# Optimization experiments

Hardware: AMD Instinct MI355X
Metric: run time of the kernel (lower is better)

## Reference

```python
import jax, jax.numpy as jnp
import numpy as np

N_NODES = 50000
N_EDGES = 800000
N_GRAPHS = 256
IN_CH = 128
HID = 256
FFN = 256
OUT = 1


def xavier(key, shape):
    fan_in, fan_out = shape[0], shape[1]
    a = jnp.sqrt(6.0 / (fan_in + fan_out))
    return jax.random.uniform(key, shape, jnp.float32, -a, a)


def setup_inputs() -> dict:
    key = jax.random.key(0)
    ks = jax.random.split(key, 12)
    x = jax.random.normal(ks[0], (N_NODES, IN_CH), jnp.float32)
    edge_index = jax.random.randint(ks[1], (2, N_EDGES), 0, N_NODES, jnp.int32)
    batch = jnp.sort(jax.random.randint(ks[2], (N_NODES,), 0, N_GRAPHS, jnp.int32))
    return {
        "x": x,
        "edge_index": edge_index,
        "batch": batch,
        # GCNConv layers (glorot weight, zero bias as in PyG reset_parameters)
        "W1": xavier(ks[3], (IN_CH, HID)), "b1": jnp.zeros((HID,), jnp.float32),
        "W2": xavier(ks[4], (HID, HID)),   "b2": jnp.zeros((HID,), jnp.float32),
        "W3": xavier(ks[5], (HID, HID)),   "b3": jnp.zeros((HID,), jnp.float32),
        # FFN: Linear(HID, FFN) then final Linear(FFN, OUT)
        "Wf": xavier(ks[6], (HID, FFN)),   "bf": jnp.zeros((FFN,), jnp.float32),
        "Wo": xavier(ks[7], (FFN, OUT)),   "bo": jnp.zeros((OUT,), jnp.float32),
    }


def _gcn_norm(edge_index, n_nodes):
    # add self-loops, compute symmetric normalization D^-1/2 (A+I) D^-1/2
    loops = jnp.arange(n_nodes, dtype=edge_index.dtype)
    row = jnp.concatenate([edge_index[0], loops])
    col = jnp.concatenate([edge_index[1], loops])
    deg = jax.ops.segment_sum(jnp.ones_like(col, jnp.float32), col, num_segments=n_nodes)
    dis = jnp.where(deg > 0, jax.lax.rsqrt(jnp.maximum(deg, 1.0)), 0.0)
    norm = dis[row] * dis[col]  # [E+N]
    return row, col, norm


def _gcn_conv(x, W, b, row, col, norm, n_nodes):
    xw = x @ W                                   # [N, H]
    msg = xw[row] * norm[:, None]                # gather + scale  [E+N, H]
    out = jax.ops.segment_sum(msg, col, num_segments=n_nodes)
    return out + b


def reference(x, edge_index, batch, W1, b1, W2, b2, W3, b3, Wf, bf, Wo, bo):
    row, col, norm = _gcn_norm(edge_index, N_NODES)
    h = jax.nn.relu(_gcn_conv(x, W1, b1, row, col, norm, N_NODES))
    h = jax.nn.relu(_gcn_conv(h, W2, b2, row, col, norm, N_NODES))
    h = jax.nn.relu(_gcn_conv(h, W3, b3, row, col, norm, N_NODES))
    # global mean pool over graphs
    counts = jax.ops.segment_sum(jnp.ones((N_NODES,), jnp.float32), batch, num_segments=N_GRAPHS)
    pooled = jax.ops.segment_sum(h, batch, num_segments=N_GRAPHS) / jnp.maximum(counts, 1.0)[:, None]
    # FFN (dropout is identity in eval mode): Linear -> ReLU -> final Linear
    g = jax.nn.relu(pooled @ Wf + bf)
    out = g @ Wo + bo
    return out
```

## Files before the change

kernel.cpp:

```cpp
#include <hip/hip_runtime.h>
#include <hip/hip_bf16.h>
#include <hip/hip_fp16.h>


#define THREADS 256
#define EPB 2048

typedef _Float16 f16x8 __attribute__((ext_vector_type(8)));
typedef float    f32x4 __attribute__((ext_vector_type(4)));
typedef unsigned short u16x8 __attribute__((ext_vector_type(8)));


__global__ void degree_goff_kernel(const int* __restrict__ col, int* __restrict__ deg, int E,
                                   const int* __restrict__ batch, int* __restrict__ goff,
                                   int N, int G) {
    int i = blockIdx.x * THREADS + threadIdx.x;
    if (i < E) atomicAdd(&deg[col[i]], 1);
    if (i < N) {
        int b1 = batch[i];
        int b0 = (i == 0) ? -1 : batch[i - 1];
        for (int g = b0 + 1; g <= b1; ++g) goff[g] = i;
        if (i == N - 1) {
            for (int g = b1 + 1; g <= G; ++g) goff[g] = N;
        }
    }
}

__global__ __launch_bounds__(256) void scanA_kernel(
    const int* __restrict__ in, int* __restrict__ out, int* __restrict__ bsum,
    float* __restrict__ dis, int n) {
    __shared__ int wsum[4];
    int i0 = blockIdx.x * 1024 + threadIdx.x * 4;
    int lane = threadIdx.x & 63, wid = threadIdx.x >> 6;
    int v0 = 0, v1 = 0, v2 = 0, v3 = 0;
    if (i0 + 3 < n) {
        int4 v = *(const int4*)&in[i0];
        v0 = v.x; v1 = v.y; v2 = v.z; v3 = v.w;
    } else {
        if (i0 + 0 < n) v0 = in[i0 + 0];
        if (i0 + 1 < n) v1 = in[i0 + 1];
        if (i0 + 2 < n) v2 = in[i0 + 2];
        if (i0 + 3 < n) v3 = in[i0 + 3];
    }
    if (i0 + 0 < n) dis[i0 + 0] = rsqrtf((float)(v0 + 1));
    if (i0 + 1 < n) dis[i0 + 1] = rsqrtf((float)(v1 + 1));
    if (i0 + 2 < n) dis[i0 + 2] = rsqrtf((float)(v2 + 1));
    if (i0 + 3 < n) dis[i0 + 3] = rsqrtf((float)(v3 + 1));
    v0 = (v0 + 7) & ~7; v1 = (v1 + 7) & ~7;
    v2 = (v2 + 7) & ~7; v3 = (v3 + 7) & ~7;
    int s = v0 + v1 + v2 + v3;
    int inc = s;
    #pragma unroll
    for (int d = 1; d < 64; d <<= 1) {
        int t = __shfl_up(inc, d);
        if (lane >= d) inc += t;
    }
    if (lane == 63) wsum[wid] = inc;
    __syncthreads();
    int add = 0;
    for (int w = 0; w < wid; ++w) add += wsum[w];
    int ex = add + inc - s;
    if (i0 + 0 < n) out[i0 + 0] = ex;
    if (i0 + 1 < n) out[i0 + 1] = ex + v0;
    if (i0 + 2 < n) out[i0 + 2] = ex + v0 + v1;
    if (i0 + 3 < n) out[i0 + 3] = ex + v0 + v1 + v2;
    if (threadIdx.x == 255) bsum[blockIdx.x] = add + inc;
}

__global__ void scanB_kernel(int* __restrict__ bsum, int* __restrict__ total_slot, int nb) {
    int lane = threadIdx.x;
    int v = (lane < nb) ? bsum[lane] : 0;
    int inc = v;
    #pragma unroll
    for (int d = 1; d < 64; d <<= 1) {
        int t = __shfl_up(inc, d);
        if (lane >= d) inc += t;
    }
    if (lane < nb) bsum[lane] = inc - v;
    if (lane == 63) *total_slot = inc;
}

__global__ __launch_bounds__(256) void padfill_x_kernel(
    const int* __restrict__ offs, const int* __restrict__ deg,
    unsigned short* __restrict__ srcs, int N) {
    int slice = blockIdx.x & 7;
    int SL = (N + 7) >> 3;
    int node = slice * SL + (int)(blockIdx.x >> 3) * THREADS + threadIdx.x;
    int nhi = min(N, slice * SL + SL);
    if (node >= nhi) return;
    int s = offs[node] + deg[node], e = offs[node + 1];
    for (int i = s; i < e; ++i) srcs[i] = (unsigned short)N;
}

__global__ __launch_bounds__(256) void csr_fill_x_kernel(
    const int* __restrict__ row, const int* __restrict__ col,
    const int* __restrict__ offs, int* __restrict__ deg,
    unsigned short* __restrict__ srcs, int E, int N) {
    int slice = blockIdx.x & 7;
    int SL = (N + 7) >> 3;
    int nlo = slice * SL;
    int nhi = min(N, nlo + SL);
    int e0 = (int)(blockIdx.x >> 3) * EPB + threadIdx.x * 8;
    if (e0 >= E) return;
    if (e0 + 8 <= E) {
        int4 c0 = *(const int4*)&col[e0];
        int4 c1 = *(const int4*)&col[e0 + 4];
        int4 r0 = *(const int4*)&row[e0];
        int4 r1 = *(const int4*)&row[e0 + 4];
        int cs[8] = {c0.x, c0.y, c0.z, c0.w, c1.x, c1.y, c1.z, c1.w};
        int rs[8] = {r0.x, r0.y, r0.z, r0.w, r1.x, r1.y, r1.z, r1.w};
        #pragma unroll
        for (int j = 0; j < 8; ++j) {
            int c = cs[j];
            if (c >= nlo && c < nhi) {
                int old = atomicSub(&deg[c], 1);
                srcs[offs[c] + old - 1] = (unsigned short)rs[j];
            }
        }
    } else {
        for (int j = 0; j < 8 && e0 + j < E; ++j) {
            int c = col[e0 + j];
            if (c >= nlo && c < nhi) {
                int old = atomicSub(&deg[c], 1);
                srcs[offs[c] + old - 1] = (unsigned short)row[e0 + j];
            }
        }
    }
}

__global__ void convert_kernel(
    int* __restrict__ offs, const int* __restrict__ bsum, int Nfix,
    const float* __restrict__ X, const float* __restrict__ dis,
    _Float16* __restrict__ Xs, int total8, int IC,
    const float* __restrict__ W1, _Float16* __restrict__ W1t, int k1,
    const float* __restrict__ W2, _Float16* __restrict__ W2t,
    const float* __restrict__ W3, _Float16* __restrict__ W3t,
    _Float16* __restrict__ Hs) {
    int i = blockIdx.x * THREADS + threadIdx.x;
    if (i < Nfix) {
        offs[i] += bsum[i >> 10];
        return;
    }
    int j = i - Nfix;
    int Ms = Nfix + 1;
    if (j < total8) {
        int idx = j * 8;
        int node = idx / IC;
        int ch0  = idx % IC;
        float d = dis[node];
        float4 a = *(const float4*)&X[idx];
        float4 b = *(const float4*)&X[idx + 4];
        f16x8 o;
        o[0] = (_Float16)(d * a.x); o[1] = (_Float16)(d * a.y);
        o[2] = (_Float16)(d * a.z); o[3] = (_Float16)(d * a.w);
        o[4] = (_Float16)(d * b.x); o[5] = (_Float16)(d * b.y);
        o[6] = (_Float16)(d * b.z); o[7] = (_Float16)(d * b.w);
        int sw = IC >> 3;
        int slice = ch0 / sw, within = ch0 % sw;
        *(f16x8*)&Xs[((size_t)slice * Ms + node) * sw + within] = o;
        return;
    }
    j -= total8;
    int n1 = k1 * 256;
    if (j < n1) {
        int k = j >> 8, n = j & 255;
        W1t[n * k1 + k] = (_Float16)W1[j];
        return;
    }
    j -= n1;
    if (j < 65536) {
        int k = j >> 8, n = j & 255;
        W2t[n * 256 + k] = (_Float16)W2[j];
        return;
    }
    j -= 65536;
    if (j < 65536) {
        int k = j >> 8, n = j & 255;
        W3t[n * 256 + k] = (_Float16)W3[j];
        return;
    }
    j -= 65536;
    {
        int swx = IC >> 3;
        int nx = 8 * swx;
        if (j < nx) {
            int slice = j / swx, wi = j % swx;
            Xs[((size_t)slice * Ms + Nfix) * swx + wi] = (_Float16)0.f;
            return;
        }
        j -= nx;
        if (j < 256) {
            int slice = j >> 5, wi = j & 31;
            Hs[((size_t)slice * Ms + Nfix) * 32 + wi] = (_Float16)0.f;
        }
    }
}


template<int CH>
__global__ __launch_bounds__(256) void aggregate_slice_kernel(
    const _Float16* __restrict__ X, const int* __restrict__ offs,
    const unsigned short* __restrict__ srcs, const float* __restrict__ dis,
    _Float16* __restrict__ A, int N) {
    constexpr int LPN = CH / 64;
    constexpr int NPB = 256 / LPN;
    int bid   = blockIdx.x;
    int slice = bid & 7;
    int tile  = bid >> 3;
    int node  = tile * NPB + threadIdx.x / LPN;
    if (node >= N) return;
    int lane = threadIdx.x % LPN;
    size_t Ms = (size_t)N + 1;
    const f16x8* Xv = (const f16x8*)X + (size_t)slice * Ms * LPN;
    f16x8 self = Xv[(size_t)node * LPN + lane];
    float acc[8], acc2[8];
    #pragma unroll
    for (int j = 0; j < 8; ++j) { acc[j] = (float)self[j]; acc2[j] = 0.f; }
    int s = offs[node], e = offs[node + 1];
    int nit = (e - s) >> 3;
    if (nit > 0) {
        const u16x8* ip = (const u16x8*)&srcs[s];
        u16x8 idx = ip[0];
        for (int it = 0; it < nit; ++it) {
            u16x8 nxt = ip[min(it + 1, nit - 1)];
            f16x8 v0 = Xv[(size_t)idx[0] * LPN + lane];
            f16x8 v1 = Xv[(size_t)idx[1] * LPN + lane];
            f16x8 v2 = Xv[(size_t)idx[2] * LPN + lane];
            f16x8 v3 = Xv[(size_t)idx[3] * LPN + lane];
            f16x8 v4 = Xv[(size_t)idx[4] * LPN + lane];
            f16x8 v5 = Xv[(size_t)idx[5] * LPN + lane];
            f16x8 v6 = Xv[(size_t)idx[6] * LPN + lane];
            f16x8 v7 = Xv[(size_t)idx[7] * LPN + lane];
            #pragma unroll
            for (int j = 0; j < 8; ++j) {
                acc[j]  += ((float)v0[j] + (float)v2[j]) + ((float)v4[j] + (float)v6[j]);
                acc2[j] += ((float)v1[j] + (float)v3[j]) + ((float)v5[j] + (float)v7[j]);
            }
            idx = nxt;
        }
    }
    float dn = dis[node];
    f16x8 o;
    #pragma unroll
    for (int j = 0; j < 8; ++j) o[j] = (_Float16)(dn * (acc[j] + acc2[j]));
    f16x8* Av = (f16x8*)A + (size_t)slice * Ms * LPN;
    __builtin_nontemporal_store(o, &Av[(size_t)node * LPN + lane]);
}


template<int K, int MODE>
__global__ __launch_bounds__(256) void gemm_as_kernel(
    const _Float16* __restrict__ A, const _Float16* __restrict__ Bt,
    const float* __restrict__ bias, const float* __restrict__ dscale,
    _Float16* __restrict__ H, float* __restrict__ pooled,
    const int* __restrict__ batch, int M, int Ms) {
    constexpr int LSA = K + 40;
    constexpr int KC = K / 32;
    constexpr int SPR = K / 8;
    constexpr int SPS = K / 64;
    constexpr int SW  = K / 8;
    __shared__ _Float16 As[64 * LSA];
    int tid = threadIdx.x;
    int m0 = blockIdx.x * 64;

    {
        constexpr int RPI = 256 / SPR;
        int r_in = tid % RPI;
        int seg  = tid / RPI;
        int slice = seg / SPS, sub = seg % SPS;
        #pragma unroll
        for (int it = 0; it < 64 / RPI; ++it) {
            int r = it * RPI + r_in;
            int gr = m0 + r;
            uint4 v = make_uint4(0, 0, 0, 0);
            if (gr < M) v = *(const uint4*)&A[((size_t)slice * Ms + gr) * SW + sub * 8];
            *(uint4*)&As[r * LSA + seg * 8] = v;
        }
    }
    __syncthreads();

    int wid = tid >> 6, lane = tid & 63;
    int l16 = lane & 15, quad = lane >> 4;
    int wn = wid * 64;

    f32x4 acc[4][4] = {};
    const _Float16* Bbase = Bt + (size_t)(wn + l16) * K + quad * 8;

    #pragma unroll
    for (int kc = 0; kc < KC; ++kc) {
        f16x8 bh[4];
        #pragma unroll
        for (int ni = 0; ni < 4; ++ni)
            bh[ni] = *(const f16x8*)&Bbase[(size_t)(ni * 16) * K + kc * 32];
        #pragma unroll
        for (int mi = 0; mi < 4; ++mi) {
            f16x8 ah = *(const f16x8*)&As[(mi * 16 + l16) * LSA + kc * 32 + quad * 8];
            #pragma unroll
            for (int ni = 0; ni < 4; ++ni)
                acc[mi][ni] = __builtin_amdgcn_mfma_f32_16x16x32_f16(ah, bh[ni], acc[mi][ni], 0, 0, 0);
        }
    }

    #pragma unroll
    for (int mi = 0; mi < 4; ++mi) {
        int rbase = m0 + mi * 16;
        int g0 = 0, g15 = 0;
        if (MODE == 2) {
            g0  = batch[min(rbase, M - 1)];
            g15 = batch[min(rbase + 15, M - 1)];
        }
        #pragma unroll
        for (int ni = 0; ni < 4; ++ni) {
            int col = wn + ni * 16 + l16;
            float bv = bias[col];
            if (MODE == 1) {
                size_t hbase = (size_t)(col >> 5) * Ms * 32 + (col & 31);
                #pragma unroll
                for (int r = 0; r < 4; ++r) {
                    int grow = rbase + quad * 4 + r;
                    if (grow < M) {
                        float v = fmaxf(acc[mi][ni][r] + bv, 0.f) * dscale[grow];
                        H[hbase + (size_t)grow * 32] = (_Float16)v;
                    }
                }
            } else {
                if (g0 == g15) {
                    float p = 0.f;
                    #pragma unroll
                    for (int r = 0; r < 4; ++r) {
                        int grow = rbase + quad * 4 + r;
                        float v = fmaxf(acc[mi][ni][r] + bv, 0.f);
                        p += (grow < M) ? v : 0.f;
                    }
                    p += __shfl_xor(p, 16);
                    p += __shfl_xor(p, 32);
                    if (quad == 0) atomicAdd(&pooled[g0 * 256 + col], p);
                } else {
                    #pragma unroll
                    for (int r = 0; r < 4; ++r) {
                        int grow = rbase + quad * 4 + r;
                        if (grow < M) {
                            float v = fmaxf(acc[mi][ni][r] + bv, 0.f);
                            atomicAdd(&pooled[batch[grow] * 256 + col], v);
                        }
                    }
                }
            }
        }
    }
}


__global__ __launch_bounds__(256) void ffn_kernel(
    const float* __restrict__ pooled, const int* __restrict__ goff,
    const float* __restrict__ Wf, const float* __restrict__ bf,
    const float* __restrict__ Wo, const float* __restrict__ bo,
    float* __restrict__ out) {
    __shared__ float p[256];
    __shared__ float red[256];
    int g = blockIdx.x, t = threadIdx.x;
    int cnt = goff[g + 1] - goff[g];
    float inv = 1.f / (float)max(cnt, 1);
    p[t] = pooled[g * 256 + t] * inv;
    __syncthreads();
    float s = bf[t];
    #pragma unroll 8
    for (int k = 0; k < 256; ++k) s = fmaf(p[k], Wf[k * 256 + t], s);
    float gv = fmaxf(s, 0.f);
    red[t] = gv * Wo[t];
    __syncthreads();
    for (int o = 128; o > 0; o >>= 1) {
        if (t < o) red[t] += red[t + o];
        __syncthreads();
    }
    if (t == 0) out[g] = red[0] + bo[0];
}


extern "C" void kernel_launch(void* const* d_in, const int* in_sizes, int n_in,
                              void* d_out, int out_size, void* d_ws, size_t ws_size,
                              hipStream_t stream) {
    const float* x   = (const float*)d_in[0];
    const int*   ei  = (const int*)d_in[1];
    const int*   bat = (const int*)d_in[2];
    const float* W1  = (const float*)d_in[3];
    const float* b1  = (const float*)d_in[4];
    const float* W2  = (const float*)d_in[5];
    const float* b2  = (const float*)d_in[6];
    const float* W3  = (const float*)d_in[7];
    const float* b3  = (const float*)d_in[8];
    const float* Wf  = (const float*)d_in[9];
    const float* bf  = (const float*)d_in[10];
    const float* Wo  = (const float*)d_in[11];
    const float* bo  = (const float*)d_in[12];
    float* out = (float*)d_out;

    const int N  = in_sizes[2];
    const int E  = in_sizes[1] / 2;
    const int IC = in_sizes[0] / N;
    const int HID = 256;
    const int G  = out_size;
    const int Ms = N + 1;
    const int* row = ei;
    const int* col = ei + E;

    char* w = (char*)d_ws;
    size_t off = 0;
    auto alloc = [&](size_t bytes) -> void* {
        void* p = w + off;
        off += (bytes + 255) & ~(size_t)255;
        return p;
    };
    int*   deg    = (int*)alloc((size_t)N * 4);
    float* pooled = (float*)alloc((size_t)G * HID * 4);
    float* dis    = (float*)alloc((size_t)N * 4);
    int*   offs   = (int*)alloc((size_t)(N + 1) * 4);
    unsigned short* srcs = (unsigned short*)alloc(((size_t)E + 7 * (size_t)N + 8) * 2);
    int*   goff   = (int*)alloc((size_t)(G + 1) * 4);
    int*   bsum   = (int*)alloc((size_t)64 * 4);
    _Float16* W1t = (_Float16*)alloc((size_t)HID * IC * 2);
    _Float16* W2t = (_Float16*)alloc((size_t)HID * HID * 2);
    _Float16* W3t = (_Float16*)alloc((size_t)HID * HID * 2);
    _Float16* Xs  = (_Float16*)alloc((size_t)Ms * IC * 2);
    _Float16* Ah  = (_Float16*)alloc((size_t)Ms * HID * 2);
    _Float16* Hs  = (_Float16*)alloc((size_t)Ms * HID * 2);
    (void)ws_size; (void)n_in;

    size_t zlen = (((size_t)N * 4 + 255) & ~(size_t)255) + (size_t)G * HID * 4;
    hipMemsetAsync(deg, 0, zlen, stream);

    int nb = (N + 1023) / 1024;
    degree_goff_kernel<<<(E + THREADS - 1) / THREADS, THREADS, 0, stream>>>(
        col, deg, E, bat, goff, N, G);
    scanA_kernel<<<nb, 256, 0, stream>>>(deg, offs, bsum, dis, N);
    scanB_kernel<<<1, 64, 0, stream>>>(bsum, &offs[N], nb);

    int total8 = N * IC / 8;
    int conv_total = N + total8 + IC * HID + HID * HID + HID * HID + 8 * (IC / 8) + 256;
    convert_kernel<<<(conv_total + THREADS - 1) / THREADS, THREADS, 0, stream>>>(
        offs, bsum, N, x, dis, Xs, total8, IC, W1, W1t, IC, W2, W2t, W3, W3t, Hs);

    int SL = (N + 7) >> 3;
    int pf_tiles = (SL + THREADS - 1) / THREADS;
    padfill_x_kernel<<<pf_tiles * 8, THREADS, 0, stream>>>(offs, deg, srcs, N);
    int cf_chunks = (E + EPB - 1) / EPB;
    csr_fill_x_kernel<<<cf_chunks * 8, THREADS, 0, stream>>>(row, col, offs, deg, srcs, E, N);

    int mtiles = (N + 63) / 64;
    int nt1 = (N + 127) / 128;
    aggregate_slice_kernel<128><<<nt1 * 8, 256, 0, stream>>>(Xs, offs, srcs, dis, Ah, N);
    gemm_as_kernel<128, 1><<<mtiles, 256, 0, stream>>>(Ah, W1t, b1, dis, Hs, nullptr, nullptr, N, Ms);
    int nt2 = (N + 63) / 64;
    aggregate_slice_kernel<256><<<nt2 * 8, 256, 0, stream>>>(Hs, offs, srcs, dis, Ah, N);
    gemm_as_kernel<256, 1><<<mtiles, 256, 0, stream>>>(Ah, W2t, b2, dis, Hs, nullptr, nullptr, N, Ms);
    aggregate_slice_kernel<256><<<nt2 * 8, 256, 0, stream>>>(Hs, offs, srcs, dis, Ah, N);
    gemm_as_kernel<256, 2><<<mtiles, 256, 0, stream>>>(Ah, W3t, b3, nullptr, nullptr, pooled, bat, N, Ms);

    ffn_kernel<<<G, 256, 0, stream>>>(pooled, goff, Wf, bf, Wo, bo, out);
}
```

Baseline: 392.2 us.

## Renumber nodes by graph and degree bucket to balance aggregation work

Adds a counting-sort permutation that groups nodes within each graph by padded-degree bucket. All node-indexed buffers (dis, offsets, CSR sources, features, batch ids) now use the permuted order. Neighbouring rows handled by one aggregation block then have similar degrees, which should reduce wavefront divergence and padding waste while keeping pooling segments contiguous. The cost is three extra small kernels plus indirect lookups during setup and CSR fill.

```diff
diff --git a/kernel.cpp b/kernel.cpp
--- a/kernel.cpp
+++ b/kernel.cpp
@@ -26,22 +26,64 @@
     }
 }
 
+__global__ void bucketcnt_kernel(const int* __restrict__ deg, const int* __restrict__ batch,
+                                 int* __restrict__ bcnt, int N) {
+    int i = blockIdx.x * THREADS + threadIdx.x;
+    if (i < N) {
+        int key = (batch[i] << 3) | min((deg[i] + 7) >> 3, 7);
+        atomicAdd(&bcnt[key], 1);
+    }
+}
+
+__global__ __launch_bounds__(256) void bucketscan_kernel(int* __restrict__ b) {
+    __shared__ int wsum[4];
+    int t = threadIdx.x, lane = t & 63, wid = t >> 6;
+    int base = t * 8;
+    int v[8];
+    #pragma unroll
+    for (int k = 0; k < 8; ++k) v[k] = b[base + k];
+    int s = 0;
+    #pragma unroll
+    for (int k = 0; k < 8; ++k) s += v[k];
+    int inc = s;
+    #pragma unroll
+    for (int d = 1; d < 64; d <<= 1) {
+        int u = __shfl_up(inc, d);
+        if (lane >= d) inc += u;
+    }
+    if (lane == 63) wsum[wid] = inc;
+    __syncthreads();
+    int add = 0;
+    for (int w = 0; w < wid; ++w) add += wsum[w];
+    int ex = add + inc - s;
+    #pragma unroll
+    for (int k = 0; k < 8; ++k) { int t2 = v[k]; b[base + k] = ex; ex += t2; }
+}
+
+__global__ void place_kernel(const int* __restrict__ deg, const int* __restrict__ batch,
+                             int* __restrict__ bcnt, int* __restrict__ perm,
+                             int* __restrict__ pinv, int* __restrict__ batch_p, int N) {
+    int i = blockIdx.x * THREADS + threadIdx.x;
+    if (i < N) {
+        int g = batch[i];
+        int key = (g << 3) | min((deg[i] + 7) >> 3, 7);
+        int pos = atomicAdd(&bcnt[key], 1);
+        perm[pos] = i; pinv[i] = pos; batch_p[pos] = g;
+    }
+}
+
 __global__ __launch_bounds__(256) void scanA_kernel(
-    const int* __restrict__ in, int* __restrict__ out, int* __restrict__ bsum,
+    const int* __restrict__ deg, const int* __restrict__ perm,
+    int* __restrict__ out, int* __restrict__ bsum,
     float* __restrict__ dis, int n) {
     __shared__ int wsum[4];
     int i0 = blockIdx.x * 1024 + threadIdx.x * 4;
     int lane = threadIdx.x & 63, wid = threadIdx.x >> 6;
     int v0 = 0, v1 = 0, v2 = 0, v3 = 0;
-    if (i0 + 3 < n) {
-        int4 v = *(const int4*)&in[i0];
-        v0 = v.x; v1 = v.y; v2 = v.z; v3 = v.w;
-    } else {
-        if (i0 + 0 < n) v0 = in[i0 + 0];
-        if (i0 + 1 < n) v1 = in[i0 + 1];
-        if (i0 + 2 < n) v2 = in[i0 + 2];
-        if (i0 + 3 < n) v3 = in[i0 + 3];
-    }
+    if (i0 + 0 < n) v0 = deg[perm[i0 + 0]];
+    if (i0 + 1 < n) v1 = deg[perm[i0 + 1]];
+    if (i0 + 2 < n) v2 = deg[perm[i0 + 2]];
+    if (i0 + 3 < n) v3 = deg[perm[i0 + 3]];
     if (i0 + 0 < n) dis[i0 + 0] = rsqrtf((float)(v0 + 1));
     if (i0 + 1 < n) dis[i0 + 1] = rsqrtf((float)(v1 + 1));
     if (i0 + 2 < n) dis[i0 + 2] = rsqrtf((float)(v2 + 1));
@@ -82,20 +124,20 @@
 
 __global__ __launch_bounds__(256) void padfill_x_kernel(
     const int* __restrict__ offs, const int* __restrict__ deg,
-    unsigned short* __restrict__ srcs, int N) {
+    const int* __restrict__ perm, unsigned short* __restrict__ srcs, int N) {
     int slice = blockIdx.x & 7;
     int SL = (N + 7) >> 3;
-    int node = slice * SL + (int)(blockIdx.x >> 3) * THREADS + threadIdx.x;
+    int p = slice * SL + (int)(blockIdx.x >> 3) * THREADS + threadIdx.x;
     int nhi = min(N, slice * SL + SL);
-    if (node >= nhi) return;
-    int s = offs[node] + deg[node], e = offs[node + 1];
+    if (p >= nhi) return;
+    int s = offs[p] + deg[perm[p]], e = offs[p + 1];
     for (int i = s; i < e; ++i) srcs[i] = (unsigned short)N;
 }
 
 __global__ __launch_bounds__(256) void csr_fill_x_kernel(
     const int* __restrict__ row, const int* __restrict__ col,
     const int* __restrict__ offs, int* __restrict__ deg,
-    unsigned short* __restrict__ srcs, int E, int N) {
+    const int* __restrict__ pinv, unsigned short* __restrict__ srcs, int E, int N) {
     int slice = blockIdx.x & 7;
     int SL = (N + 7) >> 3;
     int nlo = slice * SL;
@@ -111,18 +153,19 @@
         int rs[8] = {r0.x, r0.y, r0.z, r0.w, r1.x, r1.y, r1.z, r1.w};
         #pragma unroll
         for (int j = 0; j < 8; ++j) {
-            int c = cs[j];
-            if (c >= nlo && c < nhi) {
-                int old = atomicSub(&deg[c], 1);
-                srcs[offs[c] + old - 1] = (unsigned short)rs[j];
+            int cp = pinv[cs[j]];
+            if (cp >= nlo && cp < nhi) {
+                int old = atomicSub(&deg[cs[j]], 1);
+                srcs[offs[cp] + old - 1] = (unsigned short)pinv[rs[j]];
             }
         }
     } else {
         for (int j = 0; j < 8 && e0 + j < E; ++j) {
             int c = col[e0 + j];
-            if (c >= nlo && c < nhi) {
+            int cp = pinv[c];
+            if (cp >= nlo && cp < nhi) {
                 int old = atomicSub(&deg[c], 1);
-                srcs[offs[c] + old - 1] = (unsigned short)row[e0 + j];
+                srcs[offs[cp] + old - 1] = (unsigned short)pinv[row[e0 + j]];
             }
         }
     }
@@ -131,6 +174,7 @@
 __global__ void convert_kernel(
     int* __restrict__ offs, const int* __restrict__ bsum, int Nfix,
     const float* __restrict__ X, const float* __restrict__ dis,
+    const int* __restrict__ pinv,
     _Float16* __restrict__ Xs, int total8, int IC,
     const float* __restrict__ W1, _Float16* __restrict__ W1t, int k1,
     const float* __restrict__ W2, _Float16* __restrict__ W2t,
@@ -147,7 +191,8 @@
         int idx = j * 8;
         int node = idx / IC;
         int ch0  = idx % IC;
-        float d = dis[node];
+        int p = pinv[node];
+        float d = dis[p];
         float4 a = *(const float4*)&X[idx];
         float4 b = *(const float4*)&X[idx + 4];
         f16x8 o;
@@ -157,7 +202,7 @@
         o[6] = (_Float16)(d * b.z); o[7] = (_Float16)(d * b.w);
         int sw = IC >> 3;
         int slice = ch0 / sw, within = ch0 % sw;
-        *(f16x8*)&Xs[((size_t)slice * Ms + node) * sw + within] = o;
+        *(f16x8*)&Xs[((size_t)slice * Ms + p) * sw + within] = o;
         return;
     }
     j -= total8;
@@ -413,11 +458,15 @@
     };
     int*   deg    = (int*)alloc((size_t)N * 4);
     float* pooled = (float*)alloc((size_t)G * HID * 4);
+    int*   bcnt   = (int*)alloc((size_t)2048 * 4);
     float* dis    = (float*)alloc((size_t)N * 4);
     int*   offs   = (int*)alloc((size_t)(N + 1) * 4);
     unsigned short* srcs = (unsigned short*)alloc(((size_t)E + 7 * (size_t)N + 8) * 2);
     int*   goff   = (int*)alloc((size_t)(G + 1) * 4);
     int*   bsum   = (int*)alloc((size_t)64 * 4);
+    int*   perm   = (int*)alloc((size_t)N * 4);
+    int*   pinv   = (int*)alloc((size_t)N * 4);
+    int*   batch_p= (int*)alloc((size_t)N * 4);
     _Float16* W1t = (_Float16*)alloc((size_t)HID * IC * 2);
     _Float16* W2t = (_Float16*)alloc((size_t)HID * HID * 2);
     _Float16* W3t = (_Float16*)alloc((size_t)HID * HID * 2);
@@ -426,25 +475,32 @@
     _Float16* Hs  = (_Float16*)alloc((size_t)Ms * HID * 2);
     (void)ws_size; (void)n_in;
 
-    size_t zlen = (((size_t)N * 4 + 255) & ~(size_t)255) + (size_t)G * HID * 4;
+    size_t zlen = (((size_t)N * 4 + 255) & ~(size_t)255)
+                + (((size_t)G * HID * 4 + 255) & ~(size_t)255)
+                + (size_t)2048 * 4;
     hipMemsetAsync(deg, 0, zlen, stream);
 
-    int nb = (N + 1023) / 1024;
+    int nblk = (N + THREADS - 1) / THREADS;
     degree_goff_kernel<<<(E + THREADS - 1) / THREADS, THREADS, 0, stream>>>(
         col, deg, E, bat, goff, N, G);
-    scanA_kernel<<<nb, 256, 0, stream>>>(deg, offs, bsum, dis, N);
+    bucketcnt_kernel<<<nblk, THREADS, 0, stream>>>(deg, bat, bcnt, N);
+    bucketscan_kernel<<<1, 256, 0, stream>>>(bcnt);
+    place_kernel<<<nblk, THREADS, 0, stream>>>(deg, bat, bcnt, perm, pinv, batch_p, N);
+
+    int nb = (N + 1023) / 1024;
+    scanA_kernel<<<nb, 256, 0, stream>>>(deg, perm, offs, bsum, dis, N);
     scanB_kernel<<<1, 64, 0, stream>>>(bsum, &offs[N], nb);
 
     int total8 = N * IC / 8;
     int conv_total = N + total8 + IC * HID + HID * HID + HID * HID + 8 * (IC / 8) + 256;
     convert_kernel<<<(conv_total + THREADS - 1) / THREADS, THREADS, 0, stream>>>(
-        offs, bsum, N, x, dis, Xs, total8, IC, W1, W1t, IC, W2, W2t, W3, W3t, Hs);
+        offs, bsum, N, x, dis, pinv, Xs, total8, IC, W1, W1t, IC, W2, W2t, W3, W3t, Hs);
 
     int SL = (N + 7) >> 3;
     int pf_tiles = (SL + THREADS - 1) / THREADS;
-    padfill_x_kernel<<<pf_tiles * 8, THREADS, 0, stream>>>(offs, deg, srcs, N);
+    padfill_x_kernel<<<pf_tiles * 8, THREADS, 0, stream>>>(offs, deg, perm, srcs, N);
     int cf_chunks = (E + EPB - 1) / EPB;
-    csr_fill_x_kernel<<<cf_chunks * 8, THREADS, 0, stream>>>(row, col, offs, deg, srcs, E, N);
+    csr_fill_x_kernel<<<cf_chunks * 8, THREADS, 0, stream>>>(row, col, offs, deg, pinv, srcs, E, N);
 
     int mtiles = (N + 63) / 64;
     int nt1 = (N + 127) / 128;
@@ -454,7 +510,7 @@
     aggregate_slice_kernel<256><<<nt2 * 8, 256, 0, stream>>>(Hs, offs, srcs, dis, Ah, N);
     gemm_as_kernel<256, 1><<<mtiles, 256, 0, stream>>>(Ah, W2t, b2, dis, Hs, nullptr, nullptr, N, Ms);
     aggregate_slice_kernel<256><<<nt2 * 8, 256, 0, stream>>>(Hs, offs, srcs, dis, Ah, N);
-    gemm_as_kernel<256, 2><<<mtiles, 256, 0, stream>>>(Ah, W3t, b3, nullptr, nullptr, pooled, bat, N, Ms);
+    gemm_as_kernel<256, 2><<<mtiles, 256, 0, stream>>>(Ah, W3t, b3, nullptr, nullptr, pooled, batch_p, N, Ms);
 
     ffn_kernel<<<G, 256, 0, stream>>>(pooled, goff, Wf, bf, Wo, bo, out);
 }
```

Result: slower. 424.9 us (+8.3%).

## Pre-bin edges by destination slice before CSR fill

Applied to the files above, without the earlier changes.

Adds a pass that counts edges per destination-node slice, scans the counts, and scatters packed (col,row) pairs into per-slice bins using block-local histograms. The CSR fill kernel then reads only its own slice's bin, so it no longer has each of the 8 slice groups re-read the full edge list and filter it. This costs three extra kernel launches and an extra full pass that writes and reads the edge list, and it packs node ids into 16 bits, which assumes N fits in 16 bits.

```diff
diff --git a/kernel.cpp b/kernel.cpp
--- a/kernel.cpp
+++ b/kernel.cpp
@@ -4,7 +4,6 @@
 
 
 #define THREADS 256
-#define EPB 2048
 
 typedef _Float16 f16x8 __attribute__((ext_vector_type(8)));
 typedef float    f32x4 __attribute__((ext_vector_type(4)));
@@ -80,6 +79,88 @@
     if (lane == 63) *total_slot = inc;
 }
 
+__global__ __launch_bounds__(256) void slicecnt_kernel(
+    const int* __restrict__ deg, int* __restrict__ scnt, int N) {
+    __shared__ int wsum[4];
+    int s = blockIdx.x;
+    int SL = (N + 7) >> 3;
+    int lo = s * SL, hi = min(N, lo + SL);
+    int acc = 0;
+    for (int i = lo + (int)threadIdx.x; i < hi; i += 256) acc += deg[i];
+    #pragma unroll
+    for (int d = 1; d < 64; d <<= 1) acc += __shfl_xor(acc, d);
+    int lane = threadIdx.x & 63, wid = threadIdx.x >> 6;
+    if (lane == 0) wsum[wid] = acc;
+    __syncthreads();
+    if (threadIdx.x == 0) scnt[s] = wsum[0] + wsum[1] + wsum[2] + wsum[3];
+}
+
+__global__ void scan8_kernel(const int* __restrict__ scnt, int* __restrict__ binoff,
+                             int* __restrict__ bcur) {
+    if (threadIdx.x == 0 && blockIdx.x == 0) {
+        int cum = 0;
+        for (int s = 0; s < 8; ++s) { binoff[s] = cum; bcur[s] = cum; cum += scnt[s]; }
+        binoff[8] = cum;
+    }
+}
+
+__global__ __launch_bounds__(256) void translate_bin_kernel(
+    const int* __restrict__ row, const int* __restrict__ col,
+    unsigned int* __restrict__ bins, int* __restrict__ bcur, int E, int N) {
+    __shared__ unsigned int lent[2048];
+    __shared__ int lhist[8], lbase[8], gbase[8], lpos[8];
+    int t = threadIdx.x;
+    if (t < 8) lhist[t] = 0;
+    __syncthreads();
+    int SL = (N + 7) >> 3;
+    int e0 = blockIdx.x * 2048 + t * 8;
+    unsigned int ent[8]; int sl[8];
+    int n = E - e0; if (n < 0) n = 0; if (n > 8) n = 8;
+    if (n == 8) {
+        int4 c0 = *(const int4*)&col[e0];
+        int4 c1 = *(const int4*)&col[e0 + 4];
+        int4 r0 = *(const int4*)&row[e0];
+        int4 r1 = *(const int4*)&row[e0 + 4];
+        int cs[8] = {c0.x, c0.y, c0.z, c0.w, c1.x, c1.y, c1.z, c1.w};
+        int rs[8] = {r0.x, r0.y, r0.z, r0.w, r1.x, r1.y, r1.z, r1.w};
+        #pragma unroll
+        for (int j = 0; j < 8; ++j) {
+            sl[j] = cs[j] / SL;
+            ent[j] = (unsigned int)cs[j] | ((unsigned int)rs[j] << 16);
+            atomicAdd(&lhist[sl[j]], 1);
+        }
+    } else {
+        for (int j = 0; j < n; ++j) {
+            int c = col[e0 + j], r = row[e0 + j];
+            sl[j] = c / SL;
+            ent[j] = (unsigned int)c | ((unsigned int)r << 16);
+            atomicAdd(&lhist[sl[j]], 1);
+        }
+    }
+    __syncthreads();
+    if (t == 0) {
+        int cum = 0;
+        #pragma unroll
+        for (int s = 0; s < 8; ++s) { lbase[s] = cum; cum += lhist[s]; }
+    }
+    __syncthreads();
+    if (t < 8) { gbase[t] = atomicAdd(&bcur[t], lhist[t]); lpos[t] = lbase[t]; }
+    __syncthreads();
+    for (int j = 0; j < n; ++j) {
+        int p = atomicAdd(&lpos[sl[j]], 1);
+        lent[p] = ent[j];
+    }
+    __syncthreads();
+    int total = lbase[7] + lhist[7];
+    for (int k = t; k < total; k += 256) {
+        unsigned int e = lent[k];
+        int s = 0;
+        #pragma unroll
+        for (int b = 1; b < 8; ++b) s = (k >= lbase[b]) ? b : s;
+        bins[gbase[s] + (k - lbase[s])] = e;
+    }
+}
+
 __global__ __launch_bounds__(256) void padfill_x_kernel(
     const int* __restrict__ offs, const int* __restrict__ deg,
     unsigned short* __restrict__ srcs, int N) {
@@ -92,37 +173,24 @@
     for (int i = s; i < e; ++i) srcs[i] = (unsigned short)N;
 }
 
-__global__ __launch_bounds__(256) void csr_fill_x_kernel(
-    const int* __restrict__ row, const int* __restrict__ col,
+__global__ __launch_bounds__(256) void csr_fill2_kernel(
+    const unsigned int* __restrict__ bins, const int* __restrict__ binoff,
     const int* __restrict__ offs, int* __restrict__ deg,
-    unsigned short* __restrict__ srcs, int E, int N) {
+    unsigned short* __restrict__ srcs, int CPS) {
     int slice = blockIdx.x & 7;
-    int SL = (N + 7) >> 3;
-    int nlo = slice * SL;
-    int nhi = min(N, nlo + SL);
-    int e0 = (int)(blockIdx.x >> 3) * EPB + threadIdx.x * 8;
-    if (e0 >= E) return;
-    if (e0 + 8 <= E) {
-        int4 c0 = *(const int4*)&col[e0];
-        int4 c1 = *(const int4*)&col[e0 + 4];
-        int4 r0 = *(const int4*)&row[e0];
-        int4 r1 = *(const int4*)&row[e0 + 4];
-        int cs[8] = {c0.x, c0.y, c0.z, c0.w, c1.x, c1.y, c1.z, c1.w};
-        int rs[8] = {r0.x, r0.y, r0.z, r0.w, r1.x, r1.y, r1.z, r1.w};
+    int chunk = blockIdx.x >> 3;
+    int lo = binoff[slice], hi = binoff[slice + 1];
+    for (int base = lo + chunk * 2048; base < hi; base += CPS * 2048) {
+        int i0 = base + (int)threadIdx.x * 8;
         #pragma unroll
         for (int j = 0; j < 8; ++j) {
-            int c = cs[j];
-            if (c >= nlo && c < nhi) {
+            int i = i0 + j;
+            if (i < hi) {
+                unsigned int e = bins[i];
+                int c = (int)(e & 0xffffu);
+                int r = (int)(e >> 16);
                 int old = atomicSub(&deg[c], 1);
-                srcs[offs[c] + old - 1] = (unsigned short)rs[j];
-            }
-        }
-    } else {
-        for (int j = 0; j < 8 && e0 + j < E; ++j) {
-            int c = col[e0 + j];
-            if (c >= nlo && c < nhi) {
-                int old = atomicSub(&deg[c], 1);
-                srcs[offs[c] + old - 1] = (unsigned short)row[e0 + j];
+                srcs[offs[c] + old - 1] = (unsigned short)r;
             }
         }
     }
@@ -416,6 +484,10 @@
     float* dis    = (float*)alloc((size_t)N * 4);
     int*   offs   = (int*)alloc((size_t)(N + 1) * 4);
     unsigned short* srcs = (unsigned short*)alloc(((size_t)E + 7 * (size_t)N + 8) * 2);
+    unsigned int* bins = (unsigned int*)alloc((size_t)(E + 8) * 4);
+    int*   scnt   = (int*)alloc((size_t)8 * 4);
+    int*   binoff = (int*)alloc((size_t)9 * 4);
+    int*   bcur   = (int*)alloc((size_t)8 * 4);
     int*   goff   = (int*)alloc((size_t)(G + 1) * 4);
     int*   bsum   = (int*)alloc((size_t)64 * 4);
     _Float16* W1t = (_Float16*)alloc((size_t)HID * IC * 2);
@@ -429,11 +501,17 @@
     size_t zlen = (((size_t)N * 4 + 255) & ~(size_t)255) + (size_t)G * HID * 4;
     hipMemsetAsync(deg, 0, zlen, stream);
 
-    int nb = (N + 1023) / 1024;
     degree_goff_kernel<<<(E + THREADS - 1) / THREADS, THREADS, 0, stream>>>(
         col, deg, E, bat, goff, N, G);
+
+    int nb = (N + 1023) / 1024;
     scanA_kernel<<<nb, 256, 0, stream>>>(deg, offs, bsum, dis, N);
     scanB_kernel<<<1, 64, 0, stream>>>(bsum, &offs[N], nb);
+
+    slicecnt_kernel<<<8, 256, 0, stream>>>(deg, scnt, N);
+    scan8_kernel<<<1, 64, 0, stream>>>(scnt, binoff, bcur);
+    translate_bin_kernel<<<(E + 2047) / 2048, 256, 0, stream>>>(
+        row, col, bins, bcur, E, N);
 
     int total8 = N * IC / 8;
     int conv_total = N + total8 + IC * HID + HID * HID + HID * HID + 8 * (IC / 8) + 256;
@@ -443,8 +521,8 @@
     int SL = (N + 7) >> 3;
     int pf_tiles = (SL + THREADS - 1) / THREADS;
     padfill_x_kernel<<<pf_tiles * 8, THREADS, 0, stream>>>(offs, deg, srcs, N);
-    int cf_chunks = (E + EPB - 1) / EPB;
-    csr_fill_x_kernel<<<cf_chunks * 8, THREADS, 0, stream>>>(row, col, offs, deg, srcs, E, N);
+    int CPS = (E + 8 * 2048 - 1) / (8 * 2048);
+    csr_fill2_kernel<<<CPS * 8, 256, 0, stream>>>(bins, binoff, offs, deg, srcs, CPS);
 
     int mtiles = (N + 63) / 64;
     int nt1 = (N + 127) / 128;
```

Result: slower. 410.7 us (+4.7%).
